# Kernel tuning notes

Hardware: AMD Instinct MI355X
Metric: run time of the kernel (lower is better)

Reference implementation:

```python
import jax, jax.numpy as jnp
import numpy as np

B = 8192
EPS = 1e-5  # BatchNorm eps (torch default)


def binarize(x):
    # sign binarization with straight-through estimator (matches the .data trick
    # in BinarizeConv2d/BinarizeLinear: forward sees +-1, backward sees identity)
    s = jnp.where(x >= 0, 1.0, -1.0).astype(x.dtype)
    return x + jax.lax.stop_gradient(s - x)


def conv2d(x, w, stride, pad):
    return jax.lax.conv_general_dilated(
        x, w, window_strides=stride, padding=pad,
        dimension_numbers=('NCHW', 'OIHW', 'NCHW'))


def bn(x, g, b, m, v):
    # eval-mode BatchNorm2d folded into one scale+shift per channel
    inv = g * jax.lax.rsqrt(v + EPS)
    return x * inv[None, :, None, None] + (b - m * inv)[None, :, None, None]


def maxpool_w2(x):
    # MaxPool2d(kernel=(1,2), stride=(1,2))
    return jax.lax.reduce_window(x, -jnp.inf, jax.lax.max,
                                 (1, 1, 1, 2), (1, 1, 1, 2), 'VALID')


def setup_inputs() -> dict:
    key = jax.random.key(0)
    ks = jax.random.split(key, 32)
    d = {}
    d['x'] = jax.random.normal(ks[0], (B, 1, 6, 128), jnp.float32)

    def w(k, shape):
        return jax.random.normal(k, shape, jnp.float32) * 0.05

    # conv weights (OIHW) and biases
    d['w1'] = w(ks[1], (32, 1, 1, 9));    d['b1'] = w(ks[2], (32,))
    d['w2'] = w(ks[3], (64, 32, 1, 3));   d['b2'] = w(ks[4], (64,))
    d['w3'] = w(ks[5], (128, 64, 1, 3));  d['b3'] = w(ks[6], (128,))
    d['w4'] = w(ks[7], (128, 128, 6, 1)); d['b4'] = w(ks[8], (128,))
    # BatchNorm params (gamma, beta, running_mean, running_var)
    for i, c in zip((1, 2, 3, 4), (32, 64, 128, 128)):
        kk = jax.random.split(ks[8 + i], 4)
        d[f'g{i}'] = 1.0 + 0.1 * jax.random.normal(kk[0], (c,), jnp.float32)
        d[f'be{i}'] = 0.1 * jax.random.normal(kk[1], (c,), jnp.float32)
        d[f'm{i}'] = 0.1 * jax.random.normal(kk[2], (c,), jnp.float32)
        d[f'v{i}'] = jax.random.uniform(kk[3], (c,), jnp.float32, 0.5, 1.5)
    # fc: BinarizeLinear(2048, 10)
    d['wf'] = w(ks[20], (10, 2048))
    d['bf'] = w(ks[21], (10,))
    return d


def reference(x, w1, b1, w2, b2, w3, b3, w4, b4,
              g1, be1, m1, v1, g2, be2, m2, v2,
              g3, be3, m3, v3, g4, be4, m4, v4, wf, bf):
    # block 1: first layer keeps real-valued input, binarized weights
    h = conv2d(x, binarize(w1), (1, 2), [(0, 0), (4, 4)]) + b1[None, :, None, None]
    h = jnp.clip(bn(h, g1, be1, m1, v1), -1.0, 1.0)   # Hardtanh
    h = maxpool_w2(h)                                  # [B,32,6,32]
    # block 2: binarized activations + weights
    h = conv2d(binarize(h), binarize(w2), (1, 1), [(0, 0), (1, 1)]) + b2[None, :, None, None]
    h = jnp.clip(bn(h, g2, be2, m2, v2), -1.0, 1.0)    # [B,64,6,32]
    # block 3
    h = conv2d(binarize(h), binarize(w3), (1, 1), [(0, 0), (1, 1)]) + b3[None, :, None, None]
    h = jnp.clip(bn(h, g3, be3, m3, v3), -1.0, 1.0)
    h = maxpool_w2(h)                                  # [B,128,6,16]
    # block 4: (6,1) kernel collapses H
    h = conv2d(binarize(h), binarize(w4), (1, 1), [(0, 0), (0, 0)]) + b4[None, :, None, None]
    h = jnp.clip(bn(h, g4, be4, m4, v4), -1.0, 1.0)    # [B,128,1,16]
    h = h.reshape(h.shape[0], -1)                      # [B,2048]
    return binarize(h) @ binarize(wf).T + bf           # [B,10]
```

## Files before the change

### kernel.cpp

```cpp
#include <hip/hip_runtime.h>
#include <cstdint>
#include <cstddef>
#include <math.h>

#define BATCH 8192

typedef unsigned long long u64;
typedef uint32_t u32;
typedef int v4i __attribute__((ext_vector_type(4)));
typedef int v16i __attribute__((ext_vector_type(16)));

__device__ __forceinline__ double bn_inv_d(float g, float v) {
    return (double)g * (1.0 / sqrt((double)v + 1e-5));
}
__device__ __forceinline__ double bn_shift_d(float be, float m, double iv) {
    return (double)be - (double)m * iv;
}
__device__ __forceinline__ double bn_eval_d(double conv, double B, double iv, double sh) {
    return (conv + B) * iv + sh;
}

__global__ __launch_bounds__(256) void prep_all(
    const float* w1, const float* b1, const float* w2, const float* b2,
    const float* w3, const float* b3, const float* w4, const float* b4,
    const float* wf,
    const float* g1, const float* be1, const float* m1, const float* v1,
    const float* g2, const float* be2, const float* m2, const float* v2,
    const float* g3, const float* be3, const float* m3, const float* v3,
    const float* g4, const float* be4, const float* m4, const float* v4,
    float* s1f, double* T1, u32* wt2w, int* T2,
    uint4* b3i8, int* C3, u64* wt4, int* T4, u64* wtf) {
    int t = blockIdx.x * 256 + threadIdx.x;

    if (t < 384) {
        int co = t / 12, k = t % 12;
        float val = 0.f;
        if (k < 9) {
            double iv = bn_inv_d(g1[co], v1[co]);
            float d = (iv < 0.0) ? -1.f : 1.f;
            val = ((w1[co * 9 + k] >= 0.f) ? 1.f : -1.f) * d;
        }
        s1f[t] = val;
    } else if (t < 416) {
        int co = t - 384;
        double iv = bn_inv_d(g1[co], v1[co]);
        double sh = bn_shift_d(be1[co], m1[co], iv);
        double B = (double)b1[co];
        bool flip = (iv < 0.0);
        double tt = -sh / iv - B;
        T1[co] = flip ? -tt : tt;
    } else if (t < 608) {
        int idx = t - 416;
        int co = idx / 3, kw = idx % 3;
        double iv = bn_inv_d(g2[co], v2[co]);
        bool flip = (iv < 0.0);
        u32 wb = 0;
        for (int ci = 0; ci < 32; ++ci)
            wb |= (u32)((w2[(co * 32 + ci) * 3 + kw] >= 0.f) != flip) << ci;
        wt2w[co * 4 + kw] = wb;
    } else if (t < 800) {
        int idx = t - 608;
        int co = idx & 63, cls = idx >> 6;
        double iv = bn_inv_d(g2[co], v2[co]);
        double sh = bn_shift_d(be2[co], m2[co], iv);
        double B = (double)b2[co];
        bool flip = (iv < 0.0);
        int spur = 0, nv = 3;
        if (cls == 1) { nv = 2; for (int ci = 0; ci < 32; ++ci) spur += (int)((w2[(co * 32 + ci) * 3 + 0] >= 0.f) != flip); }
        if (cls == 2) { nv = 2; for (int ci = 0; ci < 32; ++ci) spur += (int)((w2[(co * 32 + ci) * 3 + 2] >= 0.f) != flip); }
        int maxp = 32 * nv + spur;
        int T = -1;
        for (int p = 0; p <= maxp; ++p) {
            int conv = flip ? (2 * (p - spur) - 32 * nv) : (32 * nv - 2 * (p - spur));
            double y = bn_eval_d((double)conv, B, iv, sh);
            if ((y >= 0.0) && (T == p - 1)) T = p;
        }
        T2[cls * 64 + co] = T;
    } else if (t < 2336) {
        int idx = t - 800;
        int q = idx >> 7, n = idx & 127;
        double iv = bn_inv_d(g3[n], v3[n]);
        bool flip = (iv < 0.0);
        int kw = q >> 2, ci0 = (q & 3) * 16;
        u32 wd[4] = {0, 0, 0, 0};
        for (int j = 0; j < 16; ++j) {
            int ci = ci0 + j;
            bool pos = (w3[(n * 64 + ci) * 3 + kw] >= 0.f) != flip;
            u32 byte = pos ? 0x01u : 0xFFu;
            wd[j >> 2] |= byte << (8 * (j & 3));
        }
        b3i8[idx] = make_uint4(wd[0], wd[1], wd[2], wd[3]);
    } else if (t < 2464) {
        int co = t - 2336;
        double iv = bn_inv_d(g3[co], v3[co]);
        double sh = bn_shift_d(be3[co], m3[co], iv);
        double B = (double)b3[co];
        int C = 1000;
        if (iv >= 0.0) {
            for (int v = -192; v <= 192; v += 2)
                if (bn_eval_d((double)v, B, iv, sh) >= 0.0) { C = v; break; }
        } else {
            for (int v = 192; v >= -192; v -= 2)
                if (bn_eval_d((double)v, B, iv, sh) >= 0.0) { C = -v; break; }
        }
        C3[co] = C;
    } else if (t < 4000) {
        int idx = t - 2464;
        int j = idx & 1, ch = idx >> 1;
        int co = ch / 6, h = ch % 6;
        double iv = bn_inv_d(g4[co], v4[co]);
        bool flip = (iv < 0.0);
        u64 wb = 0;
        for (int cb = 0; cb < 64; ++cb) {
            int ci = j * 64 + cb;
            wb |= (u64)((w4[(co * 128 + ci) * 6 + h] >= 0.f) != flip) << cb;
        }
        wt4[idx] = wb;
    } else if (t < 4128) {
        int co = t - 4000;
        double iv = bn_inv_d(g4[co], v4[co]);
        double sh = bn_shift_d(be4[co], m4[co], iv);
        double B = (double)b4[co];
        bool flip = (iv < 0.0);
        int T = -1;
        for (int p = 0; p <= 768; ++p) {
            int conv = flip ? (2 * p - 768) : (768 - 2 * p);
            double y = bn_eval_d((double)conv, B, iv, sh);
            if ((y >= 0.0) && (T == p - 1)) T = p;
        }
        T4[co] = T;
    } else if (t < 4448) {
        int idx = t - 4128;
        int o = idx / 32, wi = idx % 32;
        u64 wb = 0;
        for (int fb = 0; fb < 64; ++fb)
            wb |= (u64)(wf[o * 2048 + wi * 64 + fb] >= 0.f) << fb;
        wtf[idx] = wb;
    }
}

#define RB 24
__global__ __launch_bounds__(256, 4) void mega_kernel(
    const float* __restrict__ x, const float4* __restrict__ s1p, const double* __restrict__ T1g,
    const uint4* __restrict__ wt2v, const int* __restrict__ T2g,
    const uint4* __restrict__ b3i8, const int* __restrict__ C3g,
    const u64* __restrict__ wt4, const int* __restrict__ T4g,
    const u64* __restrict__ wtf, const float* __restrict__ bfg,
    float* __restrict__ out) {
    __shared__ __attribute__((aligned(16))) char smem[38656];
    uint4* sB3  = (uint4*)smem;
    u32*  sLUT4 = (u32*)(smem + 24576);
    short* sC3  = (short*)(smem + 24704);
    uint4* sW2  = (uint4*)(smem + 24960);
    short* sT2  = (short*)(smem + 25984);
    float* sX   = (float*)(smem + 26368);
    u32*  sA1   = (u32*)(smem + 31872 - 1024 + 1024);
    u64*  sA2   = (u64*)(smem + 32512);
    sA1 = (u32*)(smem + 30848);
    u64*  sW4   = (u64*)smem;
    u64*  sWf   = (u64*)(smem + 12288);
    u64*  sFeat = (u64*)(smem + 24960);
    short* sT4  = (short*)(smem + 25984);
    float* sBf  = (float*)(smem + 26240);
    u32*  sA3u  = (u32*)(smem + 26368);
    u64*  sA3q  = (u64*)(smem + 26368);

    int t = threadIdx.x;
    for (int i = t; i < 1536; i += 256) sB3[i] = b3i8[i];
    if (t < 32) {
        u32 n = t & 15;
        u32 e = 0;
#pragma unroll
        for (int j = 0; j < 4; ++j)
            e |= (((n >> j) & 1) ? 0x01u : 0xFFu) << (8 * j);
        sLUT4[t] = e;
    }
    if (t < 128) sC3[t] = (short)C3g[t];
    if (t < 64) sW2[t] = wt2v[t];
    if (t < 192) sT2[t] = (short)T2g[t];

    int co = t & 31, lane = t & 63;
    float4 wa = s1p[co * 3 + 0];
    float4 wb = s1p[co * 3 + 1];
    float wc = s1p[co * 3 + 2].x;
    double w0d = (double)wa.x, w1d = (double)wa.y, w2d = (double)wa.z, w3d = (double)wa.w;
    double w4d = (double)wb.x, w5d = (double)wb.y, w6d = (double)wb.z, w7d = (double)wb.w;
    double w8d = (double)wc;
    double Tt = T1g[co];
    float Ttf = (float)Tt;

    int bh0 = blockIdx.x * RB;
#pragma unroll 1
    for (int ch = 0; ch < 3; ++ch) {
        __syncthreads();
        for (int i = t; i < 280; i += 256) {
            int r = i / 35, c = i - r * 35;
            float4 v = make_float4(0.f, 0.f, 0.f, 0.f);
            if (c >= 1 && c <= 32)
                v = *(const float4*)&x[(size_t)(bh0 + ch * 8 + r) * 128 + (c * 4 - 4)];
            *(float4*)&sX[r * 140 + c * 4] = v;
        }
        __syncthreads();
        {
            int rr = t >> 5;
            const float* xr = &sX[rr * 140];
            float4 A0 = *(const float4*)&xr[0];
            float4 A1 = *(const float4*)&xr[4];
            float4 A2 = *(const float4*)&xr[8];
            u32 myword = 0;
#pragma unroll
            for (int wp = 0; wp < 32; ++wp) {
                float s0 = 0.f, s1 = 0.f;
                s0 = fmaf(wa.x, A0.x, s0);  s1 = fmaf(wa.x, A0.z, s1);
                s0 = fmaf(wa.y, A0.y, s0);  s1 = fmaf(wa.y, A0.w, s1);
                s0 = fmaf(wa.z, A0.z, s0);  s1 = fmaf(wa.z, A1.x, s1);
                s0 = fmaf(wa.w, A0.w, s0);  s1 = fmaf(wa.w, A1.y, s1);
                s0 = fmaf(wb.x, A1.x, s0);  s1 = fmaf(wb.x, A1.z, s1);
                s0 = fmaf(wb.y, A1.y, s0);  s1 = fmaf(wb.y, A1.w, s1);
                s0 = fmaf(wb.z, A1.z, s0);  s1 = fmaf(wb.z, A2.x, s1);
                s0 = fmaf(wb.w, A1.w, s0);  s1 = fmaf(wb.w, A2.y, s1);
                s0 = fmaf(wc,   A2.x, s0);  s1 = fmaf(wc,   A2.z, s1);
                float m0 = fmaxf(s0, s1);
                bool pred = m0 >= Ttf;
                if (__any(fabsf(m0 - Ttf) <= 5e-5f)) {
                    double d0 = 0.0, d1 = 0.0;
                    d0 = fma(w0d, (double)A0.x, d0);  d1 = fma(w0d, (double)A0.z, d1);
                    d0 = fma(w1d, (double)A0.y, d0);  d1 = fma(w1d, (double)A0.w, d1);
                    d0 = fma(w2d, (double)A0.z, d0);  d1 = fma(w2d, (double)A1.x, d1);
                    d0 = fma(w3d, (double)A0.w, d0);  d1 = fma(w3d, (double)A1.y, d1);
                    d0 = fma(w4d, (double)A1.x, d0);  d1 = fma(w4d, (double)A1.z, d1);
                    d0 = fma(w5d, (double)A1.y, d0);  d1 = fma(w5d, (double)A1.w, d1);
                    d0 = fma(w6d, (double)A1.z, d0);  d1 = fma(w6d, (double)A2.x, d1);
                    d0 = fma(w7d, (double)A1.w, d0);  d1 = fma(w7d, (double)A2.y, d1);
                    d0 = fma(w8d, (double)A2.x, d0);  d1 = fma(w8d, (double)A2.z, d1);
                    pred = ((d0 > d1) ? d0 : d1) >= Tt;
                }
                u64 mk = __ballot(pred);
                u32 hw = (lane < 32) ? (u32)mk : (u32)(mk >> 32);
                if ((lane & 31) == wp) myword = hw;
                A0 = A1; A1 = A2;
                A2 = *(const float4*)&xr[4 * wp + 12];
            }
            sA1[(((t >> 6) << 1) + (lane >> 5)) * 32 + (lane & 31)] = myword;
        }
        __syncthreads();
        {
            int r = t >> 5, wp = t & 31;
            u32 am = sA1[r * 32 + wp];
            u32 al = (wp > 0) ? sA1[r * 32 + wp - 1] : 0u;
            u32 ar = (wp < 31) ? sA1[r * 32 + wp + 1] : 0u;
            const short* Tp = &sT2[(wp == 0) ? 64 : ((wp == 31) ? 128 : 0)];
            u64 word2 = 0;
#pragma unroll
            for (int c = 0; c < 64; ++c) {
                uint4 w2v = sW2[c];
                int p = __popc(al ^ w2v.x) + __popc(am ^ w2v.y) + __popc(ar ^ w2v.z);
                word2 |= (u64)(p <= (int)Tp[c]) << c;
            }
            sA2[(ch * 8 + r) * 32 + wp] = word2;
        }
    }
    __syncthreads();

    int wq = t >> 6, m = lane & 31, half = lane >> 5;
    const u32* lp = sLUT4 + (half << 4);
    const int prTab[8] = {0, 1, 4, 5, 8, 9, 12, 13};
    for (int r6 = 0; r6 < 6; ++r6) {
        int row = wq * 6 + r6;
        u64 aw = sA2[row * 32 + m];
        u64 wm1 = (m > 0) ? sA2[row * 32 + m - 1] : 0ull;
        u64 wp1 = (m < 31) ? sA2[row * 32 + m + 1] : 0ull;

        v4i A[6];
#pragma unroll
        for (int kk = 0; kk < 6; ++kk) {
            const int kw = kk >> 1;
            u64 word = (kw == 0) ? wm1 : ((kw == 1) ? aw : wp1);
            bool valid = !((kw == 0 && m == 0) || (kw == 2 && m == 31));
            int ci0 = ((kk & 1) << 5) + (half << 4);
            u32 bits = (u32)(word >> ci0) & 0xFFFFu;
            u32 b0 = lp[bits & 15];
            u32 b1 = lp[(bits >> 4) & 15];
            u32 b2 = lp[(bits >> 8) & 15];
            u32 b3v = lp[bits >> 12];
            if (!valid) { b0 = 0; b1 = 0; b2 = 0; b3v = 0; }
            union { u32 d[4]; v4i v; } u;
            u.d[0] = b0; u.d[1] = b1; u.d[2] = b2; u.d[3] = b3v;
            A[kk] = u.v;
        }
        u32 outv = 0;
#pragma unroll
        for (int nt = 0; nt < 4; ++nt) {
            v16i acc;
#pragma unroll
            for (int i = 0; i < 16; ++i) acc[i] = 0;
#pragma unroll
            for (int kk = 0; kk < 6; ++kk) {
                int q = kk * 2 + half;
                union { uint4 u4; v4i v; } bu;
                bu.u4 = sB3[q * 128 + nt * 32 + m];
                acc = __builtin_amdgcn_mfma_i32_32x32x32_i8(A[kk], bu.v, acc, 0, 0, 0);
            }
            int tc = (int)sC3[nt * 32 + m];
#pragma unroll
            for (int rp = 0; rp < 8; ++rp) {
                bool c = (acc[2 * rp] >= tc) || (acc[2 * rp + 1] >= tc);
                u64 mk = __ballot(c);
                int LA = (nt << 4) | prTab[rp];
                int LB = LA + 2;
                outv = (lane == LA) ? (u32)mk : outv;
                outv = (lane == LB) ? (u32)(mk >> 32) : outv;
            }
        }
        sA3u[row * 64 + ((lane & 15) << 2) + (lane >> 4)] = outv;
    }
    __syncthreads();

    for (int i = t; i < 1536; i += 256) sW4[i] = wt4[i];
    for (int i = t; i < 320; i += 256) sWf[i] = wtf[i];
    if (t < 128) sT4[t] = (short)T4g[t];
    if (t < 10) sBf[t] = bfg[t];
    __syncthreads();

    {
        int bb = t >> 6;
        int w = lane & 15;
        int cg = lane >> 4;
        u64 av[12];
#pragma unroll
        for (int h = 0; h < 6; ++h) {
            av[h * 2 + 0] = sA3q[(bb * 6 + h) * 32 + w * 2 + 0];
            av[h * 2 + 1] = sA3q[(bb * 6 + h) * 32 + w * 2 + 1];
        }
        u64 acc = 0;
#pragma unroll 4
        for (int c = 0; c < 32; ++c) {
            int cc = cg * 32 + c;
            const u64* wr = &sW4[cc * 12];
            int p = 0;
#pragma unroll
            for (int q = 0; q < 12; ++q) p += __popcll(av[q] ^ wr[q]);
            u64 mk = __ballot(p <= (int)sT4[cc]);
            u64 field = (mk >> (cg * 16)) & 0xFFFFull;
            acc |= field << ((c & 3) << 4);
            if ((c & 3) == 3) {
                if (w == (c >> 2)) sFeat[bb * 32 + cg * 8 + (c >> 2)] = acc;
                acc = 0;
            }
        }
    }
    __syncthreads();
    if (t < 40) {
        int fb = t / 10, o = t % 10;
        int p = 0;
#pragma unroll
        for (int wi = 0; wi < 32; ++wi) p += __popcll(sFeat[fb * 32 + wi] ^ sWf[o * 32 + wi]);
        out[(size_t)(blockIdx.x * 4 + fb) * 10 + o] = __fadd_rn((float)(2048 - 2 * p), sBf[o]);
    }
}

extern "C" void kernel_launch(void* const* d_in, const int* in_sizes, int n_in,
                              void* d_out, int out_size, void* d_ws, size_t ws_size,
                              hipStream_t stream) {
    const float* x  = (const float*)d_in[0];
    const float* w1 = (const float*)d_in[1];  const float* b1 = (const float*)d_in[2];
    const float* w2 = (const float*)d_in[3];  const float* b2 = (const float*)d_in[4];
    const float* w3 = (const float*)d_in[5];  const float* b3 = (const float*)d_in[6];
    const float* w4 = (const float*)d_in[7];  const float* b4 = (const float*)d_in[8];
    const float* g1 = (const float*)d_in[9];  const float* be1 = (const float*)d_in[10];
    const float* m1 = (const float*)d_in[11]; const float* v1 = (const float*)d_in[12];
    const float* g2 = (const float*)d_in[13]; const float* be2 = (const float*)d_in[14];
    const float* m2 = (const float*)d_in[15]; const float* v2 = (const float*)d_in[16];
    const float* g3 = (const float*)d_in[17]; const float* be3 = (const float*)d_in[18];
    const float* m3 = (const float*)d_in[19]; const float* v3 = (const float*)d_in[20];
    const float* g4 = (const float*)d_in[21]; const float* be4 = (const float*)d_in[22];
    const float* m4 = (const float*)d_in[23]; const float* v4 = (const float*)d_in[24];
    const float* wf = (const float*)d_in[25]; const float* bf = (const float*)d_in[26];
    float* out = (float*)d_out;

    char* ws = (char*)d_ws;
    uint4*  b3i8 = (uint4*) (ws + 0);
    u64*    wt4  = (u64*)   (ws + 24576);
    u64*    wtf  = (u64*)   (ws + 36864);
    u32*    wt2w = (u32*)   (ws + 39424);
    float*  s1f  = (float*) (ws + 40448);
    double* T1   = (double*)(ws + 41984);
    int*    T2   = (int*)   (ws + 42240);
    int*    C3   = (int*)   (ws + 43008);
    int*    T4   = (int*)   (ws + 43520);

    prep_all<<<18, 256, 0, stream>>>(w1, b1, w2, b2, w3, b3, w4, b4, wf,
                                     g1, be1, m1, v1, g2, be2, m2, v2,
                                     g3, be3, m3, v3, g4, be4, m4, v4,
                                     s1f, T1, wt2w, T2, b3i8, C3, wt4, T4, wtf);

    mega_kernel<<<(BATCH * 6) / RB, 256, 0, stream>>>(
        x, (const float4*)s1f, T1, (const uint4*)wt2w, T2, b3i8, C3,
        wt4, T4, wtf, bf, out);
}
```

Baseline: 266.9 us.

## Read weights from global memory to shrink LDS and raise occupancy

Stops staging the layer-3 MFMA B operands, layer-4 weights and fc weights in shared memory and reads them straight from global (cached) memory instead. This shrinks the LDS footprint from about 38 KB to about 15 KB per block, and launch bounds are raised to 8 blocks per CU so more waves can be resident. The prep kernel's linear threshold scans become binary searches. The cost is more global/L1/L2 traffic and latency inside the MFMA and popcount loops, plus tighter register limits that could cause spills.

New measurement: 383.4 us. 43.6% more time.

```diff
diff --git a/kernel.cpp b/kernel.cpp
--- a/kernel.cpp
+++ b/kernel.cpp
@@ -18,6 +18,18 @@
 }
 __device__ __forceinline__ double bn_eval_d(double conv, double B, double iv, double sh) {
     return (conv + B) * iv + sh;
+}
+
+template <typename F>
+__device__ __forceinline__ int max_p_nonneg(F y, int maxp) {
+    if (!(y(0) >= 0.0)) return -1;
+    if (y(maxp) >= 0.0) return maxp;
+    int lo = 0, hi = maxp;
+    while (hi - lo > 1) {
+        int mid = (lo + hi) >> 1;
+        if (y(mid) >= 0.0) lo = mid; else hi = mid;
+    }
+    return lo;
 }
 
 __global__ __launch_bounds__(256) void prep_all(
@@ -69,13 +81,11 @@
         if (cls == 1) { nv = 2; for (int ci = 0; ci < 32; ++ci) spur += (int)((w2[(co * 32 + ci) * 3 + 0] >= 0.f) != flip); }
         if (cls == 2) { nv = 2; for (int ci = 0; ci < 32; ++ci) spur += (int)((w2[(co * 32 + ci) * 3 + 2] >= 0.f) != flip); }
         int maxp = 32 * nv + spur;
-        int T = -1;
-        for (int p = 0; p <= maxp; ++p) {
+        auto y = [&](int p) {
             int conv = flip ? (2 * (p - spur) - 32 * nv) : (32 * nv - 2 * (p - spur));
-            double y = bn_eval_d((double)conv, B, iv, sh);
-            if ((y >= 0.0) && (T == p - 1)) T = p;
-        }
-        T2[cls * 64 + co] = T;
+            return bn_eval_d((double)conv, B, iv, sh);
+        };
+        T2[cls * 64 + co] = max_p_nonneg(y, maxp);
     } else if (t < 2336) {
         int idx = t - 800;
         int q = idx >> 7, n = idx & 127;
@@ -95,13 +105,30 @@
         double iv = bn_inv_d(g3[co], v3[co]);
         double sh = bn_shift_d(be3[co], m3[co], iv);
         double B = (double)b3[co];
+        auto y = [&](int v) { return bn_eval_d((double)v, B, iv, sh); };
         int C = 1000;
         if (iv >= 0.0) {
-            for (int v = -192; v <= 192; v += 2)
-                if (bn_eval_d((double)v, B, iv, sh) >= 0.0) { C = v; break; }
+            if (y(192) >= 0.0) {
+                if (y(-192) >= 0.0) C = -192;
+                else {
+                    int lo = 0, hi = 192;
+                    while (hi - lo > 1) {
+                        int mid = (lo + hi) >> 1;
+                        if (y(-192 + 2 * mid) >= 0.0) hi = mid; else lo = mid;
+                    }
+                    C = -192 + 2 * hi;
+                }
+            }
         } else {
-            for (int v = 192; v >= -192; v -= 2)
-                if (bn_eval_d((double)v, B, iv, sh) >= 0.0) { C = -v; break; }
+            if (y(192) >= 0.0) C = -192;
+            else if (y(-192) >= 0.0) {
+                int lo = 0, hi = 192;
+                while (hi - lo > 1) {
+                    int mid = (lo + hi) >> 1;
+                    if (y(-192 + 2 * mid) >= 0.0) lo = mid; else hi = mid;
+                }
+                C = -(-192 + 2 * lo);
+            }
         }
         C3[co] = C;
     } else if (t < 4000) {
@@ -122,13 +149,11 @@
         double sh = bn_shift_d(be4[co], m4[co], iv);
         double B = (double)b4[co];
         bool flip = (iv < 0.0);
-        int T = -1;
-        for (int p = 0; p <= 768; ++p) {
+        auto y = [&](int p) {
             int conv = flip ? (2 * p - 768) : (768 - 2 * p);
-            double y = bn_eval_d((double)conv, B, iv, sh);
-            if ((y >= 0.0) && (T == p - 1)) T = p;
-        }
-        T4[co] = T;
+            return bn_eval_d((double)conv, B, iv, sh);
+        };
+        T4[co] = max_p_nonneg(y, 768);
     } else if (t < 4448) {
         int idx = t - 4128;
         int o = idx / 32, wi = idx % 32;
@@ -140,33 +165,28 @@
 }
 
 #define RB 24
-__global__ __launch_bounds__(256, 4) void mega_kernel(
+__global__ __launch_bounds__(256, 8) void mega_kernel(
     const float* __restrict__ x, const float4* __restrict__ s1p, const double* __restrict__ T1g,
     const uint4* __restrict__ wt2v, const int* __restrict__ T2g,
     const uint4* __restrict__ b3i8, const int* __restrict__ C3g,
     const u64* __restrict__ wt4, const int* __restrict__ T4g,
     const u64* __restrict__ wtf, const float* __restrict__ bfg,
     float* __restrict__ out) {
-    __shared__ __attribute__((aligned(16))) char smem[38656];
-    uint4* sB3  = (uint4*)smem;
-    u32*  sLUT4 = (u32*)(smem + 24576);
-    short* sC3  = (short*)(smem + 24704);
-    uint4* sW2  = (uint4*)(smem + 24960);
-    short* sT2  = (short*)(smem + 25984);
-    float* sX   = (float*)(smem + 26368);
-    u32*  sA1   = (u32*)(smem + 31872 - 1024 + 1024);
-    u64*  sA2   = (u64*)(smem + 32512);
-    sA1 = (u32*)(smem + 30848);
-    u64*  sW4   = (u64*)smem;
-    u64*  sWf   = (u64*)(smem + 12288);
-    u64*  sFeat = (u64*)(smem + 24960);
-    short* sT4  = (short*)(smem + 25984);
-    float* sBf  = (float*)(smem + 26240);
-    u32*  sA3u  = (u32*)(smem + 26368);
-    u64*  sA3q  = (u64*)(smem + 26368);
+    __shared__ __attribute__((aligned(16))) char smem[15488];
+    u32*  sLUT4 = (u32*)(smem + 0);
+    short* sC3  = (short*)(smem + 128);
+    uint4* sW2  = (uint4*)(smem + 384);
+    short* sT2  = (short*)(smem + 1408);
+    short* sT4  = (short*)(smem + 1792);
+    float* sBf  = (float*)(smem + 2048);
+    u64*  sFeat = (u64*)(smem + 2176);
+    float* sX   = (float*)(smem + 3200);
+    u32*  sA1   = (u32*)(smem + 7680);
+    u32*  sA3u  = (u32*)(smem + 3200);
+    u64*  sA3q  = (u64*)(smem + 3200);
+    u64*  sA2   = (u64*)(smem + 9344);
 
     int t = threadIdx.x;
-    for (int i = t; i < 1536; i += 256) sB3[i] = b3i8[i];
     if (t < 32) {
         u32 n = t & 15;
         u32 e = 0;
@@ -178,6 +198,8 @@
     if (t < 128) sC3[t] = (short)C3g[t];
     if (t < 64) sW2[t] = wt2v[t];
     if (t < 192) sT2[t] = (short)T2g[t];
+    if (t < 128) sT4[t] = (short)T4g[t];
+    if (t < 10) sBf[t] = bfg[t];
 
     int co = t & 31, lane = t & 63;
     float4 wa = s1p[co * 3 + 0];
@@ -298,7 +320,7 @@
             for (int kk = 0; kk < 6; ++kk) {
                 int q = kk * 2 + half;
                 union { uint4 u4; v4i v; } bu;
-                bu.u4 = sB3[q * 128 + nt * 32 + m];
+                bu.u4 = b3i8[q * 128 + nt * 32 + m];
                 acc = __builtin_amdgcn_mfma_i32_32x32x32_i8(A[kk], bu.v, acc, 0, 0, 0);
             }
             int tc = (int)sC3[nt * 32 + m];
@@ -316,12 +338,6 @@
     }
     __syncthreads();
 
-    for (int i = t; i < 1536; i += 256) sW4[i] = wt4[i];
-    for (int i = t; i < 320; i += 256) sWf[i] = wtf[i];
-    if (t < 128) sT4[t] = (short)T4g[t];
-    if (t < 10) sBf[t] = bfg[t];
-    __syncthreads();
-
     {
         int bb = t >> 6;
         int w = lane & 15;
@@ -336,7 +352,7 @@
 #pragma unroll 4
         for (int c = 0; c < 32; ++c) {
             int cc = cg * 32 + c;
-            const u64* wr = &sW4[cc * 12];
+            const u64* wr = &wt4[cc * 12];
             int p = 0;
 #pragma unroll
             for (int q = 0; q < 12; ++q) p += __popcll(av[q] ^ wr[q]);
@@ -354,7 +370,7 @@
         int fb = t / 10, o = t % 10;
         int p = 0;
 #pragma unroll
-        for (int wi = 0; wi < 32; ++wi) p += __popcll(sFeat[fb * 32 + wi] ^ sWf[o * 32 + wi]);
+        for (int wi = 0; wi < 32; ++wi) p += __popcll(sFeat[fb * 32 + wi] ^ wtf[o * 32 + wi]);
         out[(size_t)(blockIdx.x * 4 + fb) * 10 + o] = __fadd_rn((float)(2048 - 2 * p), sBf[o]);
     }
 }
```
